# Performance work log

Hardware: AMD Instinct MI355X
Metric: run time of the kernel (lower is better)

## Reference

```python
import jax, jax.numpy as jnp
import numpy as np

N = 50000      # nodes
T = 4          # snapshots
F_IN = 128     # in_channels
H_DIM = 128    # hidden_channels
E = 800000     # edges per snapshot
K = 3          # Chebyshev order


def _edge_norm(src, dst, n):
    # PyG ChebConv sym normalization with lambda_max=2.0:
    # L_hat = L - I = -D^{-1/2} A D^{-1/2}  (diagonal of L_hat is 0)
    ones = jnp.ones(src.shape[0], jnp.float32)
    deg = jax.ops.segment_sum(ones, src, num_segments=n)
    dinv = jnp.where(deg > 0, jax.lax.rsqrt(deg), 0.0)
    return -dinv[src] * dinv[dst]


def _cheb_conv(x, src, dst, w, W, b):
    # x:(N,Fi), W:(K,Fi,Fo), b:(Fo,). Tx_0=x, Tx_1=L_hat x, Tx_k=2 L_hat Tx_{k-1} - Tx_{k-2}
    n = x.shape[0]

    def prop(t):  # sparse matmul L_hat @ t via gather-scale-scatter
        return jax.ops.segment_sum(w[:, None] * t[src], dst, num_segments=n)

    Tx0 = x
    out = Tx0 @ W[0]
    Tx1 = prop(Tx0)
    out = out + Tx1 @ W[1]
    for k in range(2, K):
        Tx2 = 2.0 * prop(Tx1) - Tx0
        out = out + Tx2 @ W[k]
        Tx0, Tx1 = Tx1, Tx2
    return out + b


def setup_inputs() -> dict:
    key = jax.random.key(0)
    ks = jax.random.split(key, 12)
    x = jax.random.normal(ks[0], (T, N, F_IN), jnp.float32)
    edge_index = jax.random.randint(ks[1], (T, 2, E), 0, N, dtype=jnp.int64)

    def w(k, fi, fo):
        return jax.random.normal(k, (K, fi, fo), jnp.float32) * 0.05

    inp = {
        "x": x, "edge_index": edge_index,
        "Wxz": w(ks[2], F_IN, H_DIM), "Whz": w(ks[3], H_DIM, H_DIM),
        "Wxr": w(ks[4], F_IN, H_DIM), "Whr": w(ks[5], H_DIM, H_DIM),
        "Wxh": w(ks[6], F_IN, H_DIM), "Whh": w(ks[7], H_DIM, H_DIM),
        "bxz": jnp.zeros(H_DIM, jnp.float32), "bhz": jnp.zeros(H_DIM, jnp.float32),
        "bxr": jnp.zeros(H_DIM, jnp.float32), "bhr": jnp.zeros(H_DIM, jnp.float32),
        "bxh": jnp.zeros(H_DIM, jnp.float32), "bhh": jnp.zeros(H_DIM, jnp.float32),
        "Wd1": jax.random.normal(ks[8], (H_DIM, H_DIM), jnp.float32) * 0.05,
        "bd1": jnp.zeros(H_DIM, jnp.float32),
        "Wd2": jax.random.normal(ks[9], (H_DIM, F_IN), jnp.float32) * 0.05,
        "bd2": jnp.zeros(F_IN, jnp.float32),
    }
    return inp


def reference(x, edge_index, Wxz, Whz, Wxr, Whr, Wxh, Whh,
              bxz, bhz, bxr, bhr, bxh, bhh, Wd1, bd1, Wd2, bd2):
    n = x.shape[1]

    def step(H, inp):
        xt, ei = inp
        src, dst = ei[0], ei[1]
        w = _edge_norm(src, dst, n)
        Z = jax.nn.sigmoid(_cheb_conv(xt, src, dst, w, Wxz, bxz)
                           + _cheb_conv(H, src, dst, w, Whz, bhz))
        R = jax.nn.sigmoid(_cheb_conv(xt, src, dst, w, Wxr, bxr)
                           + _cheb_conv(H, src, dst, w, Whr, bhr))
        Ht = jnp.tanh(_cheb_conv(xt, src, dst, w, Wxh, bxh)
                      + _cheb_conv(H * R, src, dst, w, Whh, bhh))
        H = Z * H + (1.0 - Z) * Ht
        return H, None

    H0 = jnp.zeros((n, H_DIM), x.dtype)
    H, _ = jax.lax.scan(step, H0, (x, edge_index))
    # decoder (dropout is identity at inference)
    x_pred = jax.nn.relu(H @ Wd1 + bd1) @ Wd2 + bd2
    return x_pred, H
```

## Files before the change

kernel.cpp:

```cpp
#include <hip/hip_runtime.h>
#include <math.h>

#define NN 50000
#define TT 4
#define FF 128
#define EE 800000
#define NSEG 4
#define BINSEG 12500
#define NCH 32
#define CHUNK 25000
#define NCH2 128
#define CH2 6250
#define NB2 64
#define CB 782
#define SMAX 13568

typedef __attribute__((ext_vector_type(8))) short bf8_t;
typedef __attribute__((ext_vector_type(4))) float f4_t;
typedef __attribute__((ext_vector_type(8))) ushort us8;

__device__ inline ushort f2bf(float f){
  union { float f; unsigned u; } v; v.f = f;
  unsigned u = v.u;
  unsigned r = (u + 0x7fff + ((u>>16)&1)) >> 16;
  return (ushort)r;
}
__device__ inline float lo16(unsigned u){ union{unsigned u;float f;}v; v.u=u<<16; return v.f; }
__device__ inline float hi16(unsigned u){ union{unsigned u;float f;}v; v.u=u&0xffff0000u; return v.f; }
__device__ inline unsigned packbf(float x, float y){
  return (unsigned)f2bf(x) | ((unsigned)f2bf(y)<<16);
}
__device__ inline float sigm(float x){ return 1.f/(1.f+expf(-x)); }

__global__ void k_cast4(const float* __restrict__ in, ushort* __restrict__ outp, int n4){
  int i = blockIdx.x*256 + threadIdx.x;
  if(i<n4){
    float4 v = ((const float4*)in)[i];
    ushort4 o; o.x=f2bf(v.x); o.y=f2bf(v.y); o.z=f2bf(v.z); o.w=f2bf(v.w);
    ((ushort4*)outp)[i]=o;
  }
}
__global__ void k_bias(const float* bxz, const float* bhz, const float* bxr,
                       const float* bhr, const float* bxh, const float* bhh,
                       float* __restrict__ bz, float* __restrict__ br, float* __restrict__ bh){
  int i = threadIdx.x;
  int c = i & 127, s = i >> 7;
  if(s==0) bz[c]=bxz[c]+bhz[c];
  else if(s==1) br[c]=bxr[c]+bhr[c];
  else bh[c]=bxh[c]+bhh[c];
}

__global__ __launch_bounds__(256) void k_hist(const int* __restrict__ ei,
                                              int* __restrict__ part){
  int c = blockIdx.x, seg = blockIdx.y, t = blockIdx.z;
  const int* keys = ei + (size_t)t*2*EE;
  __shared__ int h[BINSEG];
  for(int i=threadIdx.x;i<BINSEG;i+=256) h[i]=0;
  __syncthreads();
  int base = seg*BINSEG;
  int e0 = c*CHUNK, e1 = e0+CHUNK;
  for(int e=e0+threadIdx.x; e<e1; e+=256){
    int k = keys[e] - base;
    if((unsigned)k < (unsigned)BINSEG) atomicAdd(&h[k],1);
  }
  __syncthreads();
  int* dp = part + ((((size_t)t)*NSEG + seg)*NCH + c)*BINSEG;
  for(int i=threadIdx.x;i<BINSEG;i+=256) dp[i]=h[i];
}
__global__ void k_merge(const int* __restrict__ part, float* __restrict__ dinv4){
  int t = blockIdx.y;
  int n = blockIdx.x*256 + threadIdx.x;
  if(n>=NN) return;
  int seg = n / BINSEG, b = n - seg*BINSEG;
  const int* p = part + ((((size_t)t)*NSEG + seg)*NCH)*BINSEG + b;
  int s = 0;
  #pragma unroll
  for(int c=0;c<NCH;++c) s += p[(size_t)c*BINSEG];
  dinv4[(size_t)t*NN + n] = s>0 ? rsqrtf((float)s) : 0.f;
}

__global__ __launch_bounds__(256) void k_ccount(const int* __restrict__ ei,
                                                int* __restrict__ ccnt){
  int c = blockIdx.x, t = blockIdx.y;
  const int* dst = ei + (size_t)t*2*EE + EE;
  __shared__ int h[NB2];
  if(threadIdx.x<NB2) h[threadIdx.x]=0;
  __syncthreads();
  int e0 = c*CH2, e1 = e0+CH2;
  for(int e=e0+threadIdx.x; e<e1; e+=256) atomicAdd(&h[dst[e]/CB],1);
  __syncthreads();
  if(threadIdx.x<NB2) ccnt[((size_t)t*NB2 + threadIdx.x)*NCH2 + c] = h[threadIdx.x];
}
__global__ __launch_bounds__(128) void k_cscan(const int* __restrict__ ccnt,
                        int* __restrict__ Abase, int* __restrict__ Bbase,
                        int* __restrict__ tot){
  int t = blockIdx.x, tid = threadIdx.x;
  __shared__ int st[NB2];
  __shared__ int sb[NB2];
  const int* cc = ccnt + (size_t)t*NB2*NCH2;
  if(tid<NB2){
    int s=0;
    for(int c=0;c<NCH2;++c) s += cc[tid*NCH2+c];
    st[tid]=s;
  }
  __syncthreads();
  if(tid==0){
    int run=0;
    for(int b=0;b<NB2;++b){ sb[b]=run; run+=st[b]; }
  }
  __syncthreads();
  if(tid<NB2){
    Bbase[t*NB2+tid]=sb[tid];
    tot[t*NB2+tid]=st[tid];
    int run = sb[tid];
    int* ab = Abase + ((size_t)t*NB2 + tid)*NCH2;
    for(int c=0;c<NCH2;++c){ ab[c]=run; run+=cc[tid*NCH2+c]; }
  }
}
__global__ __launch_bounds__(256) void k_part(const int* __restrict__ ei,
                        const int* __restrict__ Abase, unsigned* __restrict__ staging){
  int c = blockIdx.x, t = blockIdx.y;
  const int* src = ei + (size_t)t*2*EE;
  const int* dst = src + EE;
  unsigned* stg = staging + (size_t)t*EE;
  const int* ab = Abase + (size_t)t*NB2*NCH2;
  __shared__ int h[NB2];
  if(threadIdx.x<NB2) h[threadIdx.x]=0;
  __syncthreads();
  int e0 = c*CH2, e1 = e0+CH2;
  for(int e=e0+threadIdx.x; e<e1; e+=256){
    int s=src[e], d=dst[e];
    int b = d/CB, dl = d - b*CB;
    int r = atomicAdd(&h[b],1);
    stg[ab[b*NCH2 + c] + r] = ((unsigned)dl<<16) | (unsigned)s;
  }
}
__global__ __launch_bounds__(256) void k_sortb(const unsigned* __restrict__ staging,
                        const int* __restrict__ Bbase, const int* __restrict__ tot,
                        const float* __restrict__ dinv4, int2* __restrict__ meta4,
                        int* __restrict__ offs4){
  int b = blockIdx.x, t = blockIdx.y, tid = threadIdx.x;
  __shared__ int cnt[784];
  __shared__ int sd[256];
  __shared__ unsigned sorted[SMAX];
  int sA = Bbase[t*NB2+b];
  int nb = tot[t*NB2+b];
  const unsigned* stg = staging + (size_t)t*EE + sA;
  const float* dinv = dinv4 + (size_t)t*NN;
  int* offs = offs4 + (size_t)t*(NN+1);
  int2* meta = meta4 + (size_t)t*EE + sA;
  for(int i=tid;i<784;i+=256) cnt[i]=0;
  __syncthreads();
  for(int i=tid;i<nb;i+=256) atomicAdd(&cnt[stg[i]>>16],1);
  __syncthreads();
  int runS = 0;
  for(int b0=0;b0<1024;b0+=256){
    int idx=b0+tid;
    int v = (idx<784)?cnt[idx]:0;
    __syncthreads();
    sd[tid]=v; __syncthreads();
    for(int off=1;off<256;off<<=1){
      int u=(tid>=off)?sd[tid-off]:0; __syncthreads();
      sd[tid]+=u; __syncthreads();
    }
    int incl = sd[tid];
    int tc = sd[255];
    if(idx<784) cnt[idx] = incl - v + runS;
    runS += tc;
    __syncthreads();
  }
  for(int dl=tid; dl<CB; dl+=256){
    int n = b*CB + dl;
    if(n<=NN) offs[n] = sA + cnt[dl];
  }
  __syncthreads();
  for(int i=tid;i<nb;i+=256){
    unsigned v = stg[i];
    int r = atomicAdd(&cnt[v>>16],1);
    if(r<SMAX) sorted[r]=v;
  }
  __syncthreads();
  for(int i=tid;i<nb;i+=256){
    if(i>=SMAX) break;
    unsigned v = sorted[i];
    int s = v & 0xFFFF;
    int d = b*CB + (v>>16);
    int2 m; m.x = s; m.y = __float_as_int(-dinv[s]*dinv[d]);
    meta[i]=m;
  }
}

__global__ void k_spmm2(const int* __restrict__ offs, const int2* __restrict__ meta,
                        const ushort* __restrict__ Xa, const ushort* __restrict__ Xb,
                        ushort* __restrict__ outA, ushort* __restrict__ outB){
  int wid = threadIdx.x>>6, lane = threadIdx.x&63;
  int row = blockIdx.x*4+wid;
  if(row>=NN) return;
  int beg = offs[row], end = offs[row+1];
  const unsigned* XA = (const unsigned*)Xa;
  const unsigned* XB = (const unsigned*)Xb;
  float ax=0.f, ay=0.f, bx=0.f, by=0.f;
  int e = beg;
  for(; e+3<end; e+=4){
    int2 p0=meta[e+0], p1=meta[e+1], p2=meta[e+2], p3=meta[e+3];
    float w0=__int_as_float(p0.y), w1=__int_as_float(p1.y);
    float w2=__int_as_float(p2.y), w3=__int_as_float(p3.y);
    unsigned a0=XA[p0.x*64+lane], a1=XA[p1.x*64+lane], a2=XA[p2.x*64+lane], a3=XA[p3.x*64+lane];
    unsigned b0=XB[p0.x*64+lane], b1=XB[p1.x*64+lane], b2=XB[p2.x*64+lane], b3=XB[p3.x*64+lane];
    ax=fmaf(w0,lo16(a0),ax); ay=fmaf(w0,hi16(a0),ay);
    ax=fmaf(w1,lo16(a1),ax); ay=fmaf(w1,hi16(a1),ay);
    ax=fmaf(w2,lo16(a2),ax); ay=fmaf(w2,hi16(a2),ay);
    ax=fmaf(w3,lo16(a3),ax); ay=fmaf(w3,hi16(a3),ay);
    bx=fmaf(w0,lo16(b0),bx); by=fmaf(w0,hi16(b0),by);
    bx=fmaf(w1,lo16(b1),bx); by=fmaf(w1,hi16(b1),by);
    bx=fmaf(w2,lo16(b2),bx); by=fmaf(w2,hi16(b2),by);
    bx=fmaf(w3,lo16(b3),bx); by=fmaf(w3,hi16(b3),by);
  }
  for(; e<end; ++e){
    int2 pm=meta[e]; float w=__int_as_float(pm.y);
    unsigned a=XA[pm.x*64+lane], b=XB[pm.x*64+lane];
    ax=fmaf(w,lo16(a),ax); ay=fmaf(w,hi16(a),ay);
    bx=fmaf(w,lo16(b),bx); by=fmaf(w,hi16(b),by);
  }
  int oi = row*64+lane;
  ((unsigned*)outA)[oi] = packbf(ax, ay);
  ((unsigned*)outB)[oi] = packbf(bx, by);
}
__global__ void k_spmm1(const int* __restrict__ offs, const int2* __restrict__ meta,
                        const ushort* __restrict__ Xa, ushort* __restrict__ outA){
  int wid = threadIdx.x>>6, lane = threadIdx.x&63;
  int row = blockIdx.x*4+wid;
  if(row>=NN) return;
  int beg = offs[row], end = offs[row+1];
  const unsigned* XA = (const unsigned*)Xa;
  float ax=0.f, ay=0.f;
  int e = beg;
  for(; e+3<end; e+=4){
    int2 p0=meta[e+0], p1=meta[e+1], p2=meta[e+2], p3=meta[e+3];
    float w0=__int_as_float(p0.y), w1=__int_as_float(p1.y);
    float w2=__int_as_float(p2.y), w3=__int_as_float(p3.y);
    unsigned a0=XA[p0.x*64+lane], a1=XA[p1.x*64+lane], a2=XA[p2.x*64+lane], a3=XA[p3.x*64+lane];
    ax=fmaf(w0,lo16(a0),ax); ay=fmaf(w0,hi16(a0),ay);
    ax=fmaf(w1,lo16(a1),ax); ay=fmaf(w1,hi16(a1),ay);
    ax=fmaf(w2,lo16(a2),ax); ay=fmaf(w2,hi16(a2),ay);
    ax=fmaf(w3,lo16(a3),ax); ay=fmaf(w3,hi16(a3),ay);
  }
  for(; e<end; ++e){
    int2 pm=meta[e]; float w=__int_as_float(pm.y);
    unsigned a=XA[pm.x*64+lane];
    ax=fmaf(w,lo16(a),ax); ay=fmaf(w,hi16(a),ay);
  }
  ((unsigned*)outA)[row*64+lane] = packbf(ax, ay);
}

__global__ __launch_bounds__(256) void k_mgemm(
    const ushort* __restrict__ A0, const ushort* __restrict__ A1,
    const ushort* __restrict__ A2, const ushort* __restrict__ A3,
    const ushort* __restrict__ A4, const ushort* __restrict__ A5,
    const ushort* __restrict__ Bt, float* __restrict__ C,
    int K, int ldb, int ngrp, int bnstep, int coloff, int beta, int nwg)
{
  __shared__ ushort As[128*64];
  __shared__ ushort Bs[128*64];
  int tid = threadIdx.x;
  int lane = tid & 63;
  int wid = tid >> 6;
  int wr = (wid>>1)*64, wc = (wid&1)*64;
  int bid = blockIdx.x;
  int q = nwg >> 3, r = nwg & 7;
  int xs = bid & 7, j = bid >> 3;
  int logical = xs*q + ((xs<r)?xs:r) + j;
  int bm = logical / ngrp;
  int bn = (logical - bm*ngrp) * bnstep;
  f4_t acc[4][4] = {};
  int srow = tid>>3, sc = tid&7;
  int lr = lane&15, lk = lane>>4;
  int nkt = K>>6;
  for(int kt=0; kt<nkt; ++kt){
    int k0 = kt<<6;
    const ushort* Ac = (k0<128)?A0:(k0<256)?A1:(k0<384)?A2:(k0<512)?A3:(k0<640)?A4:A5;
    int kloc = k0 & 127;
    #pragma unroll
    for(int p=0;p<4;++p){
      int rr = srow + p*32;
      int gr = bm*128 + rr; if(gr>=NN) gr=NN-1;
      us8 av = *(const us8*)(Ac + (size_t)gr*128 + kloc + sc*8);
      us8 bv = *(const us8*)(Bt + (size_t)(bn*128 + rr)*ldb + k0 + sc*8);
      int wo = (rr*128 + ((sc*16) ^ ((rr&7)<<4))) >> 1;
      *(us8*)(As + wo) = av;
      *(us8*)(Bs + wo) = bv;
    }
    __syncthreads();
    #pragma unroll
    for(int kk=0;kk<2;++kk){
      bf8_t af[4], bfr[4];
      int co = kk*64 + lk*16;
      #pragma unroll
      for(int m=0;m<4;++m){
        int Ra = wr + m*16 + lr;
        af[m]  = *(const bf8_t*)(As + ((Ra*128 + (co ^ ((Ra&7)<<4)))>>1));
        int Rb = wc + m*16 + lr;
        bfr[m] = *(const bf8_t*)(Bs + ((Rb*128 + (co ^ ((Rb&7)<<4)))>>1));
      }
      #pragma unroll
      for(int m=0;m<4;++m)
        #pragma unroll
        for(int n=0;n<4;++n)
          acc[m][n] = __builtin_amdgcn_mfma_f32_16x16x32_bf16(af[m], bfr[n], acc[m][n], 0,0,0);
    }
    __syncthreads();
  }
  int row0 = bm*128 + wr + lk*4;
  int col0 = coloff + bn*128 + wc + lr;
  #pragma unroll
  for(int m=0;m<4;++m){
    #pragma unroll
    for(int i=0;i<4;++i){
      int rI = row0 + m*16 + i;
      if(rI<NN){
        float* cp = C + (size_t)rI*384 + col0;
        #pragma unroll
        for(int n=0;n<4;++n){
          float v = acc[m][n][i];
          if(beta) v += cp[n*16];
          cp[n*16] = v;
        }
      }
    }
  }
}

__global__ void k_combA(const float* __restrict__ OX, const float* __restrict__ H,
                        const float* __restrict__ bz, const float* __restrict__ br,
                        float* __restrict__ Z, ushort* __restrict__ HRb){
  int i = blockIdx.x*256 + threadIdx.x;
  if(i>=NN*FF) return;
  int r = i>>7, c = i&127;
  float zv = sigm(OX[r*384+c]     + bz[c]);
  float rv = sigm(OX[r*384+128+c] + br[c]);
  float hr = H[i]*rv;
  Z[i]=zv; HRb[i]=f2bf(hr);
}
__global__ void k_combB(const float* __restrict__ OX, const float* __restrict__ Z,
                        const float* __restrict__ H, const float* __restrict__ bh,
                        float* __restrict__ Hn, ushort* __restrict__ Hnb,
                        float* __restrict__ Hout2){
  int i = blockIdx.x*256 + threadIdx.x;
  if(i>=NN*FF) return;
  int r = i>>7, c = i&127;
  float ht = tanhf(OX[r*384+256+c] + bh[c]);
  float z = Z[i];
  float hn = z*H[i] + (1.f-z)*ht;
  Hn[i] = hn; Hnb[i] = f2bf(hn);
  if(Hout2) Hout2[i] = hn;
}
__global__ void k_gru0(const float* __restrict__ OX, const float* __restrict__ bz,
                       const float* __restrict__ bh, float* __restrict__ Hn,
                       ushort* __restrict__ Hnb){
  int i = blockIdx.x*256 + threadIdx.x;
  if(i>=NN*FF) return;
  int r = i>>7, c = i&127;
  float z  = sigm(OX[r*384+c] + bz[c]);
  float ht = tanhf(OX[r*384+256+c] + bh[c]);
  float hn = (1.f - z)*ht;
  Hn[i]=hn; Hnb[i]=f2bf(hn);
}

__global__ __launch_bounds__(256) void k_gemm(
    const float* __restrict__ A0, const float* __restrict__ B, float* __restrict__ C,
    int K, int Fo, int ldc, const float* __restrict__ bias, int act){
  __shared__ float Asq[64][17];
  __shared__ float Bsq[16][64];
  int tid = threadIdx.x;
  int tx = tid & 15, ty = tid >> 4;
  int bm = blockIdx.x, bn = blockIdx.y;
  float acc[4][4] = {{0.f}};
  int lr = tid>>2, lkv = tid&3;
  int lkk = tid>>4, lcv = tid&15;
  int arow = bm*64 + lr; if(arow >= NN) arow = NN-1;
  int nkb = K>>4;
  for(int kb=0; kb<nkb; ++kb){
    int koff = kb<<4;
    float4 av = *(const float4*)(A0 + arow*128 + koff + lkv*4);
    float4 bv = *(const float4*)(B + (koff+lkk)*Fo + bn*64 + lcv*4);
    Asq[lr][lkv*4+0]=av.x; Asq[lr][lkv*4+1]=av.y; Asq[lr][lkv*4+2]=av.z; Asq[lr][lkv*4+3]=av.w;
    *(float4*)(&Bsq[lkk][lcv*4]) = bv;
    __syncthreads();
    #pragma unroll
    for(int kk=0;kk<16;++kk){
      float a0=Asq[ty*4+0][kk], a1=Asq[ty*4+1][kk], a2=Asq[ty*4+2][kk], a3=Asq[ty*4+3][kk];
      float4 b = *(const float4*)(&Bsq[kk][tx*4]);
      acc[0][0]=fmaf(a0,b.x,acc[0][0]); acc[0][1]=fmaf(a0,b.y,acc[0][1]);
      acc[0][2]=fmaf(a0,b.z,acc[0][2]); acc[0][3]=fmaf(a0,b.w,acc[0][3]);
      acc[1][0]=fmaf(a1,b.x,acc[1][0]); acc[1][1]=fmaf(a1,b.y,acc[1][1]);
      acc[1][2]=fmaf(a1,b.z,acc[1][2]); acc[1][3]=fmaf(a1,b.w,acc[1][3]);
      acc[2][0]=fmaf(a2,b.x,acc[2][0]); acc[2][1]=fmaf(a2,b.y,acc[2][1]);
      acc[2][2]=fmaf(a2,b.z,acc[2][2]); acc[2][3]=fmaf(a2,b.w,acc[2][3]);
      acc[3][0]=fmaf(a3,b.x,acc[3][0]); acc[3][1]=fmaf(a3,b.y,acc[3][1]);
      acc[3][2]=fmaf(a3,b.z,acc[3][2]); acc[3][3]=fmaf(a3,b.w,acc[3][3]);
    }
    __syncthreads();
  }
  int row0 = bm*64 + ty*4;
  int col  = bn*64 + tx*4;
  #pragma unroll
  for(int i=0;i<4;++i){
    int r = row0+i;
    if(r<NN){
      float4 v; v.x=acc[i][0]; v.y=acc[i][1]; v.z=acc[i][2]; v.w=acc[i][3];
      if(bias){ v.x+=bias[col]; v.y+=bias[col+1]; v.z+=bias[col+2]; v.w+=bias[col+3]; }
      if(act){ v.x=fmaxf(v.x,0.f); v.y=fmaxf(v.y,0.f); v.z=fmaxf(v.z,0.f); v.w=fmaxf(v.w,0.f); }
      float* cp = C + r*ldc + col;
      *(float4*)cp = v;
    }
  }
}

__global__ void k_packx(const float* __restrict__ Wxz, const float* __restrict__ Wxr,
                        const float* __restrict__ Wxh, const float* __restrict__ Whz,
                        const float* __restrict__ Whr, ushort* __restrict__ Bt){
  int i = blockIdx.x*256 + threadIdx.x;
  if(i>=384*768) return;
  int c = i/768, k = i - c*768;
  int g = c>>7, j = c&127;
  int kb = k>>7, kk = k&127;
  float v;
  int e = kk*128 + j;
  if(kb<3){
    const float* W = (g==0)?Wxz:((g==1)?Wxr:Wxh);
    v = (kb==0) ? (W[e] - W[2*16384 + e]) : (kb==1 ? W[16384 + e] : 2.f*W[2*16384 + e]);
  } else if(g<2){
    const float* W = (g==0)?Whz:Whr;
    int kb2 = kb-3;
    v = (kb2==0) ? (W[e] - W[2*16384 + e]) : (kb2==1 ? W[16384 + e] : 2.f*W[2*16384 + e]);
  } else v = 0.f;
  Bt[i] = f2bf(v);
}
__global__ void k_packh(const float* __restrict__ Whh, ushort* __restrict__ Bt){
  int i = blockIdx.x*256 + threadIdx.x;
  if(i>=128*384) return;
  int c = i/384, k = i - c*384;
  int kb = k>>7, kk = k&127;
  int e = kk*128 + c;
  float v = (kb==0) ? (Whh[e] - Whh[2*16384 + e]) : (kb==1 ? Whh[16384 + e] : 2.f*Whh[2*16384 + e]);
  Bt[i] = f2bf(v);
}

extern "C" void kernel_launch(void* const* d_in, const int* in_sizes, int n_in,
                              void* d_out, int out_size, void* d_ws, size_t ws_size,
                              hipStream_t stream) {
  const float* x   = (const float*)d_in[0];
  const int*   ei  = (const int*)d_in[1];
  const float* Wxz = (const float*)d_in[2];
  const float* Whz = (const float*)d_in[3];
  const float* Wxr = (const float*)d_in[4];
  const float* Whr = (const float*)d_in[5];
  const float* Wxh = (const float*)d_in[6];
  const float* Whh = (const float*)d_in[7];
  const float* bxz = (const float*)d_in[8];
  const float* bhz = (const float*)d_in[9];
  const float* bxr = (const float*)d_in[10];
  const float* bhr = (const float*)d_in[11];
  const float* bxh = (const float*)d_in[12];
  const float* bhh = (const float*)d_in[13];
  const float* Wd1 = (const float*)d_in[14];
  const float* bd1 = (const float*)d_in[15];
  const float* Wd2 = (const float*)d_in[16];
  const float* bd2 = (const float*)d_in[17];
  float* out = (float*)d_out;

  char* p = (char*)d_ws;
  auto alloc = [&](size_t bytes)->void*{ void* r = (void*)p; p += (bytes+255)&~(size_t)255; return r; };
  const size_t NFB  = (size_t)NN*FF*4;
  const size_t NFB2 = (size_t)NN*FF*2;
  float* Ha   = (float*)alloc(NFB);
  float* Hb   = (float*)alloc(NFB);
  float* OX   = (float*)alloc((size_t)NN*384*4);
  float* Zb   = (float*)alloc(NFB);
  ushort* xtb4= (ushort*)alloc(NFB2*TT);
  ushort* A1b = (ushort*)alloc(NFB2);
  ushort* A2b = (ushort*)alloc(NFB2);
  ushort* A3b = (ushort*)alloc(NFB2);
  ushort* A4b = (ushort*)alloc(NFB2);
  ushort* HRb = (ushort*)alloc(NFB2);
  ushort* Hab = (ushort*)alloc(NFB2);
  ushort* Hbb = (ushort*)alloc(NFB2);
  ushort* Btx = (ushort*)alloc((size_t)384*768*2);
  ushort* Bth = (ushort*)alloc((size_t)128*384*2);
  float* bzc  = (float*)alloc(128*4);
  float* brc  = (float*)alloc(128*4);
  float* bhc  = (float*)alloc(128*4);
  float* dinv4= (float*)alloc((size_t)TT*NN*4);
  int* ccnt   = (int*)alloc((size_t)TT*NB2*NCH2*4);
  int* Abase  = (int*)alloc((size_t)TT*NB2*NCH2*4);
  int* Bbase  = (int*)alloc((size_t)TT*NB2*4);
  int* tot    = (int*)alloc((size_t)TT*NB2*4);
  int* offs4  = (int*)alloc((size_t)TT*(NN+1)*4);
  int2* meta4 = (int2*)alloc((size_t)TT*EE*8);
  int* partial = (int*)Ha;
  unsigned* staging = (unsigned*)Hb;

  const int fb = (NN*FF+255)/256;
  const int sg = (NN+3)/4;
  const int MT = (NN+127)/128;

  k_packx<<<(384*768+255)/256,256,0,stream>>>(Wxz,Wxr,Wxh,Whz,Whr,Btx);
  k_packh<<<(128*384+255)/256,256,0,stream>>>(Whh,Bth);
  k_bias<<<1,384,0,stream>>>(bxz,bhz,bxr,bhr,bxh,bhh,bzc,brc,bhc);
  k_cast4<<<(TT*NN*FF/4+255)/256,256,0,stream>>>(x, xtb4, TT*NN*FF/4);
  dim3 gh(NCH, NSEG, TT);
  k_hist<<<gh,256,0,stream>>>(ei, partial);
  dim3 gm((NN+255)/256, TT);
  k_merge<<<gm,256,0,stream>>>(partial, dinv4);
  dim3 gc(NCH2, TT);
  k_ccount<<<gc,256,0,stream>>>(ei, ccnt);
  k_cscan<<<TT,128,0,stream>>>(ccnt, Abase, Bbase, tot);
  k_part<<<gc,256,0,stream>>>(ei, Abase, staging);
  dim3 gs(NB2, TT);
  k_sortb<<<gs,256,0,stream>>>(staging, Bbase, tot, dinv4, meta4, offs4);

  float* Hc = Ha; float* Hn = Hb;
  ushort* Hcb = Hab; ushort* Hnb = Hbb;
  for(int t=0;t<TT;++t){
    const ushort* xtb = xtb4 + (size_t)t*NN*FF;
    const int* offs = offs4 + (size_t)t*(NN+1);
    const int2* meta = meta4 + (size_t)t*EE;
    if(t==0){
      k_spmm1<<<sg,256,0,stream>>>(offs,meta, xtb, A1b);
      k_spmm1<<<sg,256,0,stream>>>(offs,meta, A1b, A2b);
      int nwg0 = MT*2;
      k_mgemm<<<nwg0,256,0,stream>>>(xtb,A1b,A2b,nullptr,nullptr,nullptr,
          Btx, OX, 384, 768, 2, 2, 0, 0, nwg0);
      k_gru0<<<fb,256,0,stream>>>(OX, bzc, bhc, Hn, Hnb);
    } else {
      k_spmm2<<<sg,256,0,stream>>>(offs,meta, xtb,Hcb, A1b,A3b);
      k_spmm2<<<sg,256,0,stream>>>(offs,meta, A1b,A3b, A2b,A4b);
      int nwg1 = MT*3;
      k_mgemm<<<nwg1,256,0,stream>>>(xtb,A1b,A2b,Hcb,A3b,A4b,
          Btx, OX, 768, 768, 3, 1, 0, 0, nwg1);
      k_combA<<<fb,256,0,stream>>>(OX,Hc,bzc,brc,Zb,HRb);
      k_spmm1<<<sg,256,0,stream>>>(offs,meta, HRb, A3b);
      k_spmm1<<<sg,256,0,stream>>>(offs,meta, A3b, A4b);
      int nwg3 = MT;
      k_mgemm<<<nwg3,256,0,stream>>>(HRb,A3b,A4b,nullptr,nullptr,nullptr,
          Bth, OX, 384, 384, 1, 1, 256, 1, nwg3);
      float* hout2 = (t==TT-1) ? (out + (size_t)NN*FF) : nullptr;
      k_combB<<<fb,256,0,stream>>>(OX,Zb,Hc,bhc,Hn,Hnb,hout2);
    }
    float* tmp=Hc; Hc=Hn; Hn=tmp;
    ushort* tb=Hcb; Hcb=Hnb; Hnb=tb;
  }
  dim3 gd((NN+63)/64, 2);
  k_gemm<<<gd,256,0,stream>>>(Hc, Wd1, OX, 128, 128, 128, bd1, 1);
  k_gemm<<<gd,256,0,stream>>>(OX, Wd2, out, 128, 128, 128, bd2, 0);
}
```

Baseline: 1.276 ms.

## Store gate preactivations in bf16, vectorize GRU combine, use MFMA decoder, rework sortb

The GEMM epilogue gets mode flags. Z/R gate preactivations are written as bf16 into a compact 256-column buffer and the candidate preactivation into a separate fp32 128-column buffer, replacing the 384-wide fp32 OX array. The GRU combine kernels process two columns per thread. The fp32 decoder GEMMs are replaced by the bf16 MFMA GEMM with fused bias and ReLU. k_sortb now sorts by (dst, src-segment) keys with a single scatter pass straight to global memory, which drops the shared staging array. Together these cut memory traffic and decoder cost, at the price of bf16 rounding on gate preactivations and decoder inputs.

```diff
diff --git a/kernel.cpp b/kernel.cpp
--- a/kernel.cpp
+++ b/kernel.cpp
@@ -13,7 +13,10 @@
 #define CH2 6250
 #define NB2 64
 #define CB 782
-#define SMAX 13568
+#define NSEG2 16
+#define SEGW 3125
+#define SBINS (CB*NSEG2)
+#define SCHUNK 49
 
 typedef __attribute__((ext_vector_type(8))) short bf8_t;
 typedef __attribute__((ext_vector_type(4))) float f4_t;
@@ -25,6 +28,7 @@
   unsigned r = (u + 0x7fff + ((u>>16)&1)) >> 16;
   return (ushort)r;
 }
+__device__ inline float bf2f(ushort u){ union{unsigned u;float f;}v; v.u=(unsigned)u<<16; return v.f; }
 __device__ inline float lo16(unsigned u){ union{unsigned u;float f;}v; v.u=u<<16; return v.f; }
 __device__ inline float hi16(unsigned u){ union{unsigned u;float f;}v; v.u=u&0xffff0000u; return v.f; }
 __device__ inline unsigned packbf(float x, float y){
@@ -140,53 +144,48 @@
                         const float* __restrict__ dinv4, int2* __restrict__ meta4,
                         int* __restrict__ offs4){
   int b = blockIdx.x, t = blockIdx.y, tid = threadIdx.x;
-  __shared__ int cnt[784];
-  __shared__ int sd[256];
-  __shared__ unsigned sorted[SMAX];
+  __shared__ int cnt[SBINS];
+  __shared__ int sums[256];
   int sA = Bbase[t*NB2+b];
   int nb = tot[t*NB2+b];
   const unsigned* stg = staging + (size_t)t*EE + sA;
   const float* dinv = dinv4 + (size_t)t*NN;
   int* offs = offs4 + (size_t)t*(NN+1);
   int2* meta = meta4 + (size_t)t*EE + sA;
-  for(int i=tid;i<784;i+=256) cnt[i]=0;
-  __syncthreads();
-  for(int i=tid;i<nb;i+=256) atomicAdd(&cnt[stg[i]>>16],1);
-  __syncthreads();
-  int runS = 0;
-  for(int b0=0;b0<1024;b0+=256){
-    int idx=b0+tid;
-    int v = (idx<784)?cnt[idx]:0;
-    __syncthreads();
-    sd[tid]=v; __syncthreads();
-    for(int off=1;off<256;off<<=1){
-      int u=(tid>=off)?sd[tid-off]:0; __syncthreads();
-      sd[tid]+=u; __syncthreads();
-    }
-    int incl = sd[tid];
-    int tc = sd[255];
-    if(idx<784) cnt[idx] = incl - v + runS;
-    runS += tc;
-    __syncthreads();
-  }
+  for(int i=tid;i<SBINS;i+=256) cnt[i]=0;
+  __syncthreads();
+  for(int i=tid;i<nb;i+=256){
+    unsigned v = stg[i];
+    int key = (int)(v>>16)*NSEG2 + (int)(v&0xFFFF)/SEGW;
+    atomicAdd(&cnt[key],1);
+  }
+  __syncthreads();
+  int base = tid*SCHUNK;
+  int s0 = 0;
+  for(int j=0;j<SCHUNK;++j){ int idx=base+j; if(idx<SBINS) s0+=cnt[idx]; }
+  sums[tid]=s0; __syncthreads();
+  for(int off=1;off<256;off<<=1){
+    int v=(tid>=off)?sums[tid-off]:0; __syncthreads();
+    sums[tid]+=v; __syncthreads();
+  }
+  int run = sums[tid]-s0;
+  for(int j=0;j<SCHUNK;++j){
+    int idx=base+j;
+    if(idx<SBINS){ int c=cnt[idx]; cnt[idx]=run; run+=c; }
+  }
+  __syncthreads();
   for(int dl=tid; dl<CB; dl+=256){
     int n = b*CB + dl;
-    if(n<=NN) offs[n] = sA + cnt[dl];
+    if(n<=NN) offs[n] = sA + cnt[dl*NSEG2];
   }
   __syncthreads();
   for(int i=tid;i<nb;i+=256){
     unsigned v = stg[i];
-    int r = atomicAdd(&cnt[v>>16],1);
-    if(r<SMAX) sorted[r]=v;
-  }
-  __syncthreads();
-  for(int i=tid;i<nb;i+=256){
-    if(i>=SMAX) break;
-    unsigned v = sorted[i];
-    int s = v & 0xFFFF;
-    int d = b*CB + (v>>16);
+    int key = (int)(v>>16)*NSEG2 + (int)(v&0xFFFF)/SEGW;
+    int r = atomicAdd(&cnt[key],1);
+    int s = v & 0xFFFF, d = b*CB + (v>>16);
     int2 m; m.x = s; m.y = __float_as_int(-dinv[s]*dinv[d]);
-    meta[i]=m;
+    meta[r]=m;
   }
 }
 
@@ -257,8 +256,9 @@
     const ushort* __restrict__ A0, const ushort* __restrict__ A1,
     const ushort* __restrict__ A2, const ushort* __restrict__ A3,
     const ushort* __restrict__ A4, const ushort* __restrict__ A5,
-    const ushort* __restrict__ Bt, float* __restrict__ C,
-    int K, int ldb, int ngrp, int bnstep, int coloff, int beta, int nwg)
+    const ushort* __restrict__ Bt, ushort* __restrict__ Cb, float* __restrict__ Cf,
+    int K, int ldb, int ngrp, int bnstep, int mode, int nwg,
+    const float* __restrict__ bias)
 {
   __shared__ ushort As[128*64];
   __shared__ ushort Bs[128*64];
@@ -311,109 +311,86 @@
     __syncthreads();
   }
   int row0 = bm*128 + wr + lk*4;
-  int col0 = coloff + bn*128 + wc + lr;
+  int col0 = bn*128 + wc + lr;
   #pragma unroll
   for(int m=0;m<4;++m){
     #pragma unroll
     for(int i=0;i<4;++i){
       int rI = row0 + m*16 + i;
       if(rI<NN){
-        float* cp = C + (size_t)rI*384 + col0;
         #pragma unroll
         for(int n=0;n<4;++n){
+          int c = col0 + n*16;
           float v = acc[m][n][i];
-          if(beta) v += cp[n*16];
-          cp[n*16] = v;
+          if(mode==4){
+            if(bn==2) Cf[(size_t)rI*128 + (c-256)] = v;
+            else      Cb[(size_t)rI*256 + c] = f2bf(v);
+          } else if(mode==5){
+            Cf[(size_t)rI*128 + c] += v;
+          } else if(mode==2){
+            v += bias[c]; v = fmaxf(v,0.f);
+            Cb[(size_t)rI*128 + c] = f2bf(v);
+          } else {
+            v += bias[c];
+            Cf[(size_t)rI*128 + c] = v;
+          }
         }
       }
     }
   }
 }
 
-__global__ void k_combA(const float* __restrict__ OX, const float* __restrict__ H,
+__global__ void k_combA(const ushort* __restrict__ OXb, const float* __restrict__ H,
                         const float* __restrict__ bz, const float* __restrict__ br,
                         float* __restrict__ Z, ushort* __restrict__ HRb){
   int i = blockIdx.x*256 + threadIdx.x;
-  if(i>=NN*FF) return;
-  int r = i>>7, c = i&127;
-  float zv = sigm(OX[r*384+c]     + bz[c]);
-  float rv = sigm(OX[r*384+128+c] + br[c]);
-  float hr = H[i]*rv;
-  Z[i]=zv; HRb[i]=f2bf(hr);
-}
-__global__ void k_combB(const float* __restrict__ OX, const float* __restrict__ Z,
+  if(i>=NN*64) return;
+  int rr = i>>6, c2 = (i&63)*2;
+  const unsigned* OXu = (const unsigned*)OXb;
+  unsigned zv2 = OXu[rr*128 + (c2>>1)];
+  unsigned rv2 = OXu[rr*128 + 64 + (c2>>1)];
+  float z0 = sigm(lo16(zv2)+bz[c2]),   z1 = sigm(hi16(zv2)+bz[c2+1]);
+  float r0 = sigm(lo16(rv2)+br[c2]),   r1 = sigm(hi16(rv2)+br[c2+1]);
+  float2 h = ((const float2*)H)[i];
+  float2 zz; zz.x=z0; zz.y=z1;
+  ((float2*)Z)[i] = zz;
+  ((unsigned*)HRb)[i] = packbf(h.x*r0, h.y*r1);
+}
+__global__ void k_combB(const float* __restrict__ OXh, const float* __restrict__ Z,
                         const float* __restrict__ H, const float* __restrict__ bh,
                         float* __restrict__ Hn, ushort* __restrict__ Hnb,
                         float* __restrict__ Hout2){
   int i = blockIdx.x*256 + threadIdx.x;
-  if(i>=NN*FF) return;
-  int r = i>>7, c = i&127;
-  float ht = tanhf(OX[r*384+256+c] + bh[c]);
-  float z = Z[i];
-  float hn = z*H[i] + (1.f-z)*ht;
-  Hn[i] = hn; Hnb[i] = f2bf(hn);
-  if(Hout2) Hout2[i] = hn;
-}
-__global__ void k_gru0(const float* __restrict__ OX, const float* __restrict__ bz,
-                       const float* __restrict__ bh, float* __restrict__ Hn,
-                       ushort* __restrict__ Hnb){
-  int i = blockIdx.x*256 + threadIdx.x;
-  if(i>=NN*FF) return;
-  int r = i>>7, c = i&127;
-  float z  = sigm(OX[r*384+c] + bz[c]);
-  float ht = tanhf(OX[r*384+256+c] + bh[c]);
-  float hn = (1.f - z)*ht;
-  Hn[i]=hn; Hnb[i]=f2bf(hn);
-}
-
-__global__ __launch_bounds__(256) void k_gemm(
-    const float* __restrict__ A0, const float* __restrict__ B, float* __restrict__ C,
-    int K, int Fo, int ldc, const float* __restrict__ bias, int act){
-  __shared__ float Asq[64][17];
-  __shared__ float Bsq[16][64];
-  int tid = threadIdx.x;
-  int tx = tid & 15, ty = tid >> 4;
-  int bm = blockIdx.x, bn = blockIdx.y;
-  float acc[4][4] = {{0.f}};
-  int lr = tid>>2, lkv = tid&3;
-  int lkk = tid>>4, lcv = tid&15;
-  int arow = bm*64 + lr; if(arow >= NN) arow = NN-1;
-  int nkb = K>>4;
-  for(int kb=0; kb<nkb; ++kb){
-    int koff = kb<<4;
-    float4 av = *(const float4*)(A0 + arow*128 + koff + lkv*4);
-    float4 bv = *(const float4*)(B + (koff+lkk)*Fo + bn*64 + lcv*4);
-    Asq[lr][lkv*4+0]=av.x; Asq[lr][lkv*4+1]=av.y; Asq[lr][lkv*4+2]=av.z; Asq[lr][lkv*4+3]=av.w;
-    *(float4*)(&Bsq[lkk][lcv*4]) = bv;
-    __syncthreads();
-    #pragma unroll
-    for(int kk=0;kk<16;++kk){
-      float a0=Asq[ty*4+0][kk], a1=Asq[ty*4+1][kk], a2=Asq[ty*4+2][kk], a3=Asq[ty*4+3][kk];
-      float4 b = *(const float4*)(&Bsq[kk][tx*4]);
-      acc[0][0]=fmaf(a0,b.x,acc[0][0]); acc[0][1]=fmaf(a0,b.y,acc[0][1]);
-      acc[0][2]=fmaf(a0,b.z,acc[0][2]); acc[0][3]=fmaf(a0,b.w,acc[0][3]);
-      acc[1][0]=fmaf(a1,b.x,acc[1][0]); acc[1][1]=fmaf(a1,b.y,acc[1][1]);
-      acc[1][2]=fmaf(a1,b.z,acc[1][2]); acc[1][3]=fmaf(a1,b.w,acc[1][3]);
-      acc[2][0]=fmaf(a2,b.x,acc[2][0]); acc[2][1]=fmaf(a2,b.y,acc[2][1]);
-      acc[2][2]=fmaf(a2,b.z,acc[2][2]); acc[2][3]=fmaf(a2,b.w,acc[2][3]);
-      acc[3][0]=fmaf(a3,b.x,acc[3][0]); acc[3][1]=fmaf(a3,b.y,acc[3][1]);
-      acc[3][2]=fmaf(a3,b.z,acc[3][2]); acc[3][3]=fmaf(a3,b.w,acc[3][3]);
-    }
-    __syncthreads();
-  }
-  int row0 = bm*64 + ty*4;
-  int col  = bn*64 + tx*4;
-  #pragma unroll
-  for(int i=0;i<4;++i){
-    int r = row0+i;
-    if(r<NN){
-      float4 v; v.x=acc[i][0]; v.y=acc[i][1]; v.z=acc[i][2]; v.w=acc[i][3];
-      if(bias){ v.x+=bias[col]; v.y+=bias[col+1]; v.z+=bias[col+2]; v.w+=bias[col+3]; }
-      if(act){ v.x=fmaxf(v.x,0.f); v.y=fmaxf(v.y,0.f); v.z=fmaxf(v.z,0.f); v.w=fmaxf(v.w,0.f); }
-      float* cp = C + r*ldc + col;
-      *(float4*)cp = v;
-    }
-  }
+  if(i>=NN*64) return;
+  int c2 = (i&63)*2;
+  float2 hv = ((const float2*)OXh)[i];
+  float2 z  = ((const float2*)Z)[i];
+  float2 h  = ((const float2*)H)[i];
+  float t0 = tanhf(hv.x + bh[c2]);
+  float t1 = tanhf(hv.y + bh[c2+1]);
+  float hn0 = z.x*h.x + (1.f-z.x)*t0;
+  float hn1 = z.y*h.y + (1.f-z.y)*t1;
+  float2 hn; hn.x=hn0; hn.y=hn1;
+  ((float2*)Hn)[i] = hn;
+  ((unsigned*)Hnb)[i] = packbf(hn0, hn1);
+  if(Hout2) ((float2*)Hout2)[i] = hn;
+}
+__global__ void k_gru0(const ushort* __restrict__ OXb, const float* __restrict__ OXh,
+                       const float* __restrict__ bz, const float* __restrict__ bh,
+                       float* __restrict__ Hn, ushort* __restrict__ Hnb){
+  int i = blockIdx.x*256 + threadIdx.x;
+  if(i>=NN*64) return;
+  int rr = i>>6, c2 = (i&63)*2;
+  const unsigned* OXu = (const unsigned*)OXb;
+  unsigned zv2 = OXu[rr*128 + (c2>>1)];
+  float2 hv = ((const float2*)OXh)[i];
+  float z0 = sigm(lo16(zv2)+bz[c2]),  z1 = sigm(hi16(zv2)+bz[c2+1]);
+  float t0 = tanhf(hv.x + bh[c2]);
+  float t1 = tanhf(hv.y + bh[c2+1]);
+  float hn0 = (1.f-z0)*t0, hn1 = (1.f-z1)*t1;
+  float2 hn; hn.x=hn0; hn.y=hn1;
+  ((float2*)Hn)[i] = hn;
+  ((unsigned*)Hnb)[i] = packbf(hn0, hn1);
 }
 
 __global__ void k_packx(const float* __restrict__ Wxz, const float* __restrict__ Wxr,
@@ -444,6 +421,12 @@
   int e = kk*128 + c;
   float v = (kb==0) ? (Whh[e] - Whh[2*16384 + e]) : (kb==1 ? Whh[16384 + e] : 2.f*Whh[2*16384 + e]);
   Bt[i] = f2bf(v);
+}
+__global__ void k_packd(const float* __restrict__ W, ushort* __restrict__ Bt){
+  int i = blockIdx.x*256 + threadIdx.x;
+  if(i>=128*128) return;
+  int c = i>>7, k = i&127;
+  Bt[i] = f2bf(W[k*128 + c]);
 }
 
 extern "C" void kernel_launch(void* const* d_in, const int* in_sizes, int n_in,
@@ -475,8 +458,9 @@
   const size_t NFB2 = (size_t)NN*FF*2;
   float* Ha   = (float*)alloc(NFB);
   float* Hb   = (float*)alloc(NFB);
-  float* OX   = (float*)alloc((size_t)NN*384*4);
+  float* OXh  = (float*)alloc(NFB);
   float* Zb   = (float*)alloc(NFB);
+  ushort* OXb = (ushort*)alloc((size_t)NN*256*2);
   ushort* xtb4= (ushort*)alloc(NFB2*TT);
   ushort* A1b = (ushort*)alloc(NFB2);
   ushort* A2b = (ushort*)alloc(NFB2);
@@ -487,6 +471,8 @@
   ushort* Hbb = (ushort*)alloc(NFB2);
   ushort* Btx = (ushort*)alloc((size_t)384*768*2);
   ushort* Bth = (ushort*)alloc((size_t)128*384*2);
+  ushort* Btd1= (ushort*)alloc((size_t)128*128*2);
+  ushort* Btd2= (ushort*)alloc((size_t)128*128*2);
   float* bzc  = (float*)alloc(128*4);
   float* brc  = (float*)alloc(128*4);
   float* bhc  = (float*)alloc(128*4);
@@ -500,12 +486,14 @@
   int* partial = (int*)Ha;
   unsigned* staging = (unsigned*)Hb;
 
-  const int fb = (NN*FF+255)/256;
+  const int fb2 = (NN*64+255)/256;
   const int sg = (NN+3)/4;
   const int MT = (NN+127)/128;
 
   k_packx<<<(384*768+255)/256,256,0,stream>>>(Wxz,Wxr,Wxh,Whz,Whr,Btx);
   k_packh<<<(128*384+255)/256,256,0,stream>>>(Whh,Bth);
+  k_packd<<<64,256,0,stream>>>(Wd1,Btd1);
+  k_packd<<<64,256,0,stream>>>(Wd2,Btd2);
   k_bias<<<1,384,0,stream>>>(bxz,bhz,bxr,bhr,bxh,bhh,bzc,brc,bhc);
   k_cast4<<<(TT*NN*FF/4+255)/256,256,0,stream>>>(x, xtb4, TT*NN*FF/4);
   dim3 gh(NCH, NSEG, TT);
@@ -530,27 +518,28 @@
       k_spmm1<<<sg,256,0,stream>>>(offs,meta, A1b, A2b);
       int nwg0 = MT*2;
       k_mgemm<<<nwg0,256,0,stream>>>(xtb,A1b,A2b,nullptr,nullptr,nullptr,
-          Btx, OX, 384, 768, 2, 2, 0, 0, nwg0);
-      k_gru0<<<fb,256,0,stream>>>(OX, bzc, bhc, Hn, Hnb);
+          Btx, OXb, OXh, 384, 768, 2, 2, 4, nwg0, nullptr);
+      k_gru0<<<fb2,256,0,stream>>>(OXb, OXh, bzc, bhc, Hn, Hnb);
     } else {
       k_spmm2<<<sg,256,0,stream>>>(offs,meta, xtb,Hcb, A1b,A3b);
       k_spmm2<<<sg,256,0,stream>>>(offs,meta, A1b,A3b, A2b,A4b);
       int nwg1 = MT*3;
       k_mgemm<<<nwg1,256,0,stream>>>(xtb,A1b,A2b,Hcb,A3b,A4b,
-          Btx, OX, 768, 768, 3, 1, 0, 0, nwg1);
-      k_combA<<<fb,256,0,stream>>>(OX,Hc,bzc,brc,Zb,HRb);
+          Btx, OXb, OXh, 768, 768, 3, 1, 4, nwg1, nullptr);
+      k_combA<<<fb2,256,0,stream>>>(OXb,Hc,bzc,brc,Zb,HRb);
       k_spmm1<<<sg,256,0,stream>>>(offs,meta, HRb, A3b);
       k_spmm1<<<sg,256,0,stream>>>(offs,meta, A3b, A4b);
       int nwg3 = MT;
       k_mgemm<<<nwg3,256,0,stream>>>(HRb,A3b,A4b,nullptr,nullptr,nullptr,
-          Bth, OX, 384, 384, 1, 1, 256, 1, nwg3);
+          Bth, nullptr, OXh, 384, 384, 1, 1, 5, nwg3, nullptr);
       float* hout2 = (t==TT-1) ? (out + (size_t)NN*FF) : nullptr;
-      k_combB<<<fb,256,0,stream>>>(OX,Zb,Hc,bhc,Hn,Hnb,hout2);
+      k_combB<<<fb2,256,0,stream>>>(OXh,Zb,Hc,bhc,Hn,Hnb,hout2);
     }
     float* tmp=Hc; Hc=Hn; Hn=tmp;
     ushort* tb=Hcb; Hcb=Hnb; Hnb=tb;
   }
-  dim3 gd((NN+63)/64, 2);
-  k_gemm<<<gd,256,0,stream>>>(Hc, Wd1, OX, 128, 128, 128, bd1, 1);
-  k_gemm<<<gd,256,0,stream>>>(OX, Wd2, out, 128, 128, 128, bd2, 0);
-}
+  k_mgemm<<<MT,256,0,stream>>>(Hcb,nullptr,nullptr,nullptr,nullptr,nullptr,
+      Btd1, A1b, nullptr, 128, 128, 1, 1, 2, MT, bd1);
+  k_mgemm<<<MT,256,0,stream>>>(A1b,nullptr,nullptr,nullptr,nullptr,nullptr,
+      Btd2, nullptr, out, 128, 128, 1, 1, 3, MT, bd2);
+}
```

Result: slower. 1.326 ms (+3.9%).
